# Kernel tuning notes

Hardware: AMD Instinct MI355X
Metric: run time of the kernel (lower is better)

## Reference

```python
import jax, jax.numpy as jnp
from jax import lax
import numpy as np

DIM = 256
D_STATE = 16
D_CONV = 4
EXPAND = 2
D_INNER = EXPAND * DIM          # 512
DT_RANK = (DIM + 15) // 16      # 16
EPS = 1e-5


def setup_inputs() -> dict:
    key = jax.random.key(0)
    ks = jax.random.split(key, 8)
    B, H, W = 8, 32, 32
    dt_init = 0.01  # softplus(b_dt) ~= dt_init at init (mamba-style)
    return {
        "x": jax.random.normal(ks[0], (B, DIM, H, W), jnp.float32),
        "ln_gamma": jnp.ones((DIM,), jnp.float32),
        "ln_beta": jnp.zeros((DIM,), jnp.float32),
        "W_in": jax.random.normal(ks[1], (DIM, 2 * D_INNER), jnp.float32) * 0.02,
        "conv_w": jax.random.normal(ks[2], (D_INNER, D_CONV), jnp.float32) * 0.2,
        "conv_b": jnp.zeros((D_INNER,), jnp.float32),
        "W_xproj": jax.random.normal(ks[3], (D_INNER, DT_RANK + 2 * D_STATE), jnp.float32) * 0.02,
        "W_dt": jax.random.normal(ks[4], (DT_RANK, D_INNER), jnp.float32) * 0.05,
        "b_dt": jnp.full((D_INNER,), float(np.log(np.expm1(dt_init))), jnp.float32),
        "A_log": jnp.log(jnp.broadcast_to(
            jnp.arange(1, D_STATE + 1, dtype=jnp.float32), (D_INNER, D_STATE))),
        "D_skip": jnp.ones((D_INNER,), jnp.float32),
        "W_out": jax.random.normal(ks[5], (D_INNER, DIM), jnp.float32) * 0.02,
    }


def _mamba_layer(x, ln_gamma, ln_beta, W_in, conv_w, conv_b, W_xproj,
                 W_dt, b_dt, A_log, D_skip, W_out):
    B, C, H, W = x.shape
    L = H * W
    # (B,C,H,W) -> (B, L, C)
    xf = x.transpose(0, 2, 3, 1).reshape(B, L, C)
    # LayerNorm over channel dim
    mu = xf.mean(-1, keepdims=True)
    var = ((xf - mu) ** 2).mean(-1, keepdims=True)
    xn = (xf - mu) * lax.rsqrt(var + EPS) * ln_gamma + ln_beta
    # in_proj -> u (ssm branch) and z (gate branch)
    xz = xn @ W_in                              # [B, L, 2*D_INNER]
    u, z = xz[..., :D_INNER], xz[..., D_INNER:]
    # causal depthwise conv1d over L, then SiLU
    uc = u.transpose(0, 2, 1)                   # [B, D_INNER, L]
    uc = lax.conv_general_dilated(
        uc, conv_w[:, None, :], window_strides=(1,),
        padding=[(D_CONV - 1, 0)], feature_group_count=D_INNER)
    u2 = jax.nn.silu(uc + conv_b[None, :, None]).transpose(0, 2, 1)  # [B, L, D_INNER]
    # input-dependent dt, B, C
    dbc = u2 @ W_xproj                          # [B, L, DT_RANK + 2*D_STATE]
    dt = jax.nn.softplus(dbc[..., :DT_RANK] @ W_dt + b_dt)            # [B, L, D_INNER]
    Bm = dbc[..., DT_RANK:DT_RANK + D_STATE]    # [B, L, D_STATE]
    Cm = dbc[..., DT_RANK + D_STATE:]           # [B, L, D_STATE]
    A = -jnp.exp(A_log)                         # [D_INNER, D_STATE]

    def step(h, ins):
        dt_t, B_t, C_t, u_t = ins               # [B,Din], [B,S], [B,S], [B,Din]
        dA = jnp.exp(dt_t[:, :, None] * A)      # [B, Din, S]
        h = dA * h + dt_t[:, :, None] * B_t[:, None, :] * u_t[:, :, None]
        y = jnp.einsum('bds,bs->bd', h, C_t)
        return h, y

    h0 = jnp.zeros((B, D_INNER, D_STATE), xf.dtype)
    xs = (dt.transpose(1, 0, 2), Bm.transpose(1, 0, 2),
          Cm.transpose(1, 0, 2), u2.transpose(1, 0, 2))
    _, ys = lax.scan(step, h0, xs)              # ys: [L, B, D_INNER]
    y = ys.transpose(1, 0, 2) + u2 * D_skip     # skip connection D*u
    y = y * jax.nn.silu(z)                      # gate
    o = y @ W_out                               # [B, L, C]
    return o.reshape(B, H, W, C).transpose(0, 3, 1, 2) + x


def reference(x, ln_gamma, ln_beta, W_in, conv_w, conv_b, W_xproj,
              W_dt, b_dt, A_log, D_skip, W_out):
    return _mamba_layer(x, ln_gamma, ln_beta, W_in, conv_w, conv_b, W_xproj,
                        W_dt, b_dt, A_log, D_skip, W_out)
```

## Files before the change

kernel.cpp:

```cpp
#include <hip/hip_runtime.h>
#include <hip/hip_bf16.h>
#include <math.h>

#define DIMC   256
#define DI     512
#define DS     16
#define DTR    16
#define NX     48
#define BATCH  8
#define LSEQ   1024
#define MROWS  8192
#define CHUNK  64
#define NC     (LSEQ / CHUNK)

typedef __attribute__((ext_vector_type(8))) short short8;
typedef __attribute__((ext_vector_type(4))) float f32x4;

__device__ __forceinline__ unsigned short f2bf(float v) {
  __hip_bfloat16 h = __float2bfloat16(v);
  return *reinterpret_cast<unsigned short*>(&h);
}
__device__ __forceinline__ float bf2f(unsigned short u) {
  return __int_as_float(((int)u) << 16);
}

__device__ __forceinline__ void load_lds16(const void* g, void* l) {
  __builtin_amdgcn_global_load_lds(
      (const __attribute__((address_space(1))) unsigned int*)g,
      (__attribute__((address_space(3))) unsigned int*)l, 16, 0, 0);
}

__device__ __forceinline__ float dpp_sum16(float v) {
  float t;
  t = __int_as_float(__builtin_amdgcn_mov_dpp(__float_as_int(v), 0xB1,  0xF, 0xF, true)); v += t;
  t = __int_as_float(__builtin_amdgcn_mov_dpp(__float_as_int(v), 0x4E,  0xF, 0xF, true)); v += t;
  t = __int_as_float(__builtin_amdgcn_mov_dpp(__float_as_int(v), 0x141, 0xF, 0xF, true)); v += t;
  t = __int_as_float(__builtin_amdgcn_mov_dpp(__float_as_int(v), 0x140, 0xF, 0xF, true)); v += t;
  return v;
}

__global__ __launch_bounds__(256) void prologue(const float* __restrict__ W_in,
                                                const float* __restrict__ W_out,
                                                const float* __restrict__ W_xproj,
                                                const float* __restrict__ W_dt,
                                                const float* __restrict__ x,
                                                const float* __restrict__ gamma,
                                                const float* __restrict__ beta,
                                                unsigned short* __restrict__ Wib,
                                                unsigned short* __restrict__ Wob,
                                                unsigned short* __restrict__ Wxpb,
                                                unsigned short* __restrict__ Wdtb,
                                                unsigned short* __restrict__ xnb) {
  __shared__ float sx[DIMC][67];
  __shared__ float smean[64], srs[64];
  const int blk = blockIdx.x, tid = threadIdx.x;
  if (blk < 384) {
    float (*t)[67] = sx;
    const float* W; unsigned short* Wt; int K, N, bx, by;
    if (blk < 256) { W = W_in;  Wt = Wib; K = DIMC; N = 1024; bx = blk & 31; by = blk >> 5; }
    else           { W = W_out; Wt = Wob; K = DI;   N = DIMC; bx = (blk - 256) & 7; by = (blk - 256) >> 3; }
    int n0 = bx * 32, k0 = by * 32;
    int tx = tid & 31, ty = tid >> 5;
    for (int i = ty; i < 32; i += 8) t[i][tx] = W[(size_t)(k0 + i) * N + n0 + tx];
    __syncthreads();
    for (int i = ty; i < 32; i += 8)
      Wt[(size_t)(n0 + i) * K + k0 + tx] = f2bf(t[tx][i]);
    return;
  }
  if (blk < 512) {
    int idx = (blk - 384) * 256 + tid;
    int n = idx >> 9, k = idx & 511;
    Wxpb[idx] = (n < NX) ? f2bf(W_xproj[(size_t)k * NX + n]) : (unsigned short)0;
    return;
  }
  if (blk < 576) {
    int idx = (blk - 512) * 256 + tid;
    int n = idx >> 5, k = idx & 31;
    Wdtb[idx] = (k < DTR) ? f2bf(W_dt[(size_t)k * DI + n]) : (unsigned short)0;
    return;
  }
  const int lb = blk - 576;
  const int b = lb >> 4, l0 = (lb & 15) * 64;
  {
    const int cbase = tid >> 2;
    const int lp = (tid & 3) * 16;
#pragma unroll
    for (int cg = 0; cg < 4; ++cg) {
      const int c = cg * 64 + cbase;
      const float* p = x + ((size_t)b * DIMC + c) * LSEQ + l0 + lp;
#pragma unroll
      for (int q = 0; q < 4; ++q) {
        float4 v = *(const float4*)(p + q * 4);
        sx[c][lp + q * 4 + 0] = v.x;
        sx[c][lp + q * 4 + 1] = v.y;
        sx[c][lp + q * 4 + 2] = v.z;
        sx[c][lp + q * 4 + 3] = v.w;
      }
    }
  }
  __syncthreads();
  {
    const int lane = tid & 63, w = tid >> 6;
    const int l = (w << 4) + (lane & 15);
    const int quad = lane >> 4;
    float sum = 0.f, sq = 0.f;
#pragma unroll 8
    for (int cc = 0; cc < 64; ++cc) {
      float v = sx[quad * 64 + cc][l];
      sum += v; sq += v * v;
    }
    sum += __shfl_xor(sum, 16); sq += __shfl_xor(sq, 16);
    sum += __shfl_xor(sum, 32); sq += __shfl_xor(sq, 32);
    if (quad == 0) {
      float mean = sum * (1.f / 256.f);
      float var  = sq * (1.f / 256.f) - mean * mean;
      smean[l] = mean; srs[l] = rsqrtf(var + 1e-5f);
    }
  }
  __syncthreads();
  {
    const float gg = gamma[tid], bb = beta[tid];
    const size_t base = ((size_t)b * LSEQ + l0) * DIMC + tid;
#pragma unroll 4
    for (int ll = 0; ll < 64; ++ll) {
      float v = (sx[tid][ll] - smean[ll]) * srs[ll] * gg + bb;
      xnb[base + (size_t)ll * DIMC] = f2bf(v);
    }
  }
}

__global__ __launch_bounds__(256) void gemm_bf16_128(const unsigned short* __restrict__ A,
                                                     const unsigned short* __restrict__ Bt,
                                                     unsigned short* __restrict__ Cb,
                                                     int M, int N, int K) {
  __shared__ unsigned short As[128][32];
  __shared__ unsigned short Bs[128][32];
  const int tid = threadIdx.x;
  const int lane = tid & 63, wave = tid >> 6;
  const int wm = wave >> 1, wn = wave & 1;
  const int quad = lane >> 4, l16 = lane & 15;
  const int m0 = blockIdx.y * 128, n0 = blockIdx.x * 128;

  f32x4 acc[4][4];
#pragma unroll
  for (int i = 0; i < 4; ++i)
#pragma unroll
    for (int j = 0; j < 4; ++j) acc[i][j] = (f32x4){0.f, 0.f, 0.f, 0.f};

  for (int k0 = 0; k0 < K; k0 += 32) {
#pragma unroll
    for (int q = 0; q < 2; ++q) {
      int id = q * 256 + tid;
      int row = id >> 2, c = id & 3;
      load_lds16(A + (size_t)(m0 + row) * K + k0 + c * 8,
                 (char*)&As[0][0] + (size_t)(q * 256 + wave * 64) * 16);
    }
#pragma unroll
    for (int q = 0; q < 2; ++q) {
      int id = q * 256 + tid;
      int row = id >> 2, c = id & 3;
      load_lds16(Bt + (size_t)(n0 + row) * K + k0 + c * 8,
                 (char*)&Bs[0][0] + (size_t)(q * 256 + wave * 64) * 16);
    }
    __syncthreads();
    short8 af[4], bfr[4];
#pragma unroll
    for (int i = 0; i < 4; ++i)
      af[i] = *(const short8*)&As[wm * 64 + i * 16 + l16][quad * 8];
#pragma unroll
    for (int j = 0; j < 4; ++j)
      bfr[j] = *(const short8*)&Bs[wn * 64 + j * 16 + l16][quad * 8];
#pragma unroll
    for (int i = 0; i < 4; ++i)
#pragma unroll
      for (int j = 0; j < 4; ++j)
        acc[i][j] = __builtin_amdgcn_mfma_f32_16x16x32_bf16(af[i], bfr[j], acc[i][j], 0, 0, 0);
    __syncthreads();
  }

#pragma unroll
  for (int i = 0; i < 4; ++i) {
    int rowb = wm * 64 + i * 16 + quad * 4;
#pragma unroll
    for (int j = 0; j < 4; ++j) {
      int n = n0 + wn * 64 + j * 16 + l16;
#pragma unroll
      for (int r = 0; r < 4; ++r)
        Cb[(size_t)(m0 + rowb + r) * N + n] = f2bf(acc[i][j][r]);
    }
  }
}

#define GTM 128
#define GTN 64
#define GBK 32
__global__ __launch_bounds__(256) void gemm_bf16(const unsigned short* __restrict__ A,
                                                 const unsigned short* __restrict__ Bt,
                                                 void* __restrict__ Cout,
                                                 int M, int N, int K, int mode,
                                                 const float* __restrict__ X) {
  __shared__ unsigned short As[GTM][GBK];
  __shared__ unsigned short Bs[GTN][GBK];
  const int tid = threadIdx.x;
  const int lane = tid & 63, wave = tid >> 6;
  const int wm = wave >> 1, wn = wave & 1;
  const int quad = lane >> 4, l16 = lane & 15;
  const int m0 = blockIdx.y * GTM, n0 = blockIdx.x * GTN;

  f32x4 acc[4][2];
#pragma unroll
  for (int i = 0; i < 4; ++i)
#pragma unroll
    for (int j = 0; j < 2; ++j) acc[i][j] = (f32x4){0.f, 0.f, 0.f, 0.f};

  for (int k0 = 0; k0 < K; k0 += GBK) {
#pragma unroll
    for (int q = 0; q < 2; ++q) {
      int id = q * 256 + tid;
      int row = id >> 2, c = id & 3;
      load_lds16(A + (size_t)(m0 + row) * K + k0 + c * 8,
                 (char*)&As[0][0] + (size_t)(q * 256 + wave * 64) * 16);
    }
    {
      int row = tid >> 2, c = tid & 3;
      load_lds16(Bt + (size_t)(n0 + row) * K + k0 + c * 8,
                 (char*)&Bs[0][0] + (size_t)(wave * 64) * 16);
    }
    __syncthreads();
    short8 af[4], bfrag[2];
#pragma unroll
    for (int i = 0; i < 4; ++i)
      af[i] = *(const short8*)&As[wm * 64 + i * 16 + l16][quad * 8];
#pragma unroll
    for (int j = 0; j < 2; ++j)
      bfrag[j] = *(const short8*)&Bs[wn * 32 + j * 16 + l16][quad * 8];
#pragma unroll
    for (int i = 0; i < 4; ++i)
#pragma unroll
      for (int j = 0; j < 2; ++j)
        acc[i][j] = __builtin_amdgcn_mfma_f32_16x16x32_bf16(af[i], bfrag[j], acc[i][j], 0, 0, 0);
    __syncthreads();
  }

  if (mode == 2) {
    unsigned short* Cb = (unsigned short*)Cout;
#pragma unroll
    for (int i = 0; i < 4; ++i) {
      int rowb = wm * 64 + i * 16 + quad * 4;
#pragma unroll
      for (int j = 0; j < 2; ++j) {
        int n = n0 + wn * 32 + j * 16 + l16;
#pragma unroll
        for (int r = 0; r < 4; ++r)
          Cb[(size_t)(m0 + rowb + r) * N + n] = f2bf(acc[i][j][r]);
      }
    }
  } else {
    float* C = (float*)Cout;
#pragma unroll
    for (int i = 0; i < 4; ++i) {
      int m = m0 + wm * 64 + i * 16 + quad * 4;
      int b = m >> 10, l = m & 1023;
#pragma unroll
      for (int j = 0; j < 2; ++j) {
        int n = n0 + wn * 32 + j * 16 + l16;
        size_t o = (size_t)b * (DIMC * LSEQ) + (size_t)n * LSEQ + l;
        f32x4 xv = *(const f32x4*)(X + o);
        f32x4 rv = acc[i][j] + xv;
        *(f32x4*)(C + o) = rv;
      }
    }
  }
}

__global__ __launch_bounds__(256) void conv_xproj_dt(
    const unsigned short* __restrict__ xzb,
    const float* __restrict__ conv_w,
    const float* __restrict__ conv_b,
    const unsigned short* __restrict__ Wxpb,
    const unsigned short* __restrict__ Wdtb,
    const float* __restrict__ b_dt,
    float* __restrict__ dbcBC,
    unsigned int* __restrict__ dtu) {
  __shared__ unsigned short sxz[19][512];
  __shared__ unsigned short su[16][512 + 8];
  __shared__ unsigned short sdbc[16][40];
  const int m0 = blockIdx.x * 16;
  const int l0 = m0 & 1023;
  const int tid = threadIdx.x, lane = tid & 63, w = tid >> 6;
  const int quad = lane >> 4, l16 = lane & 15;

#pragma unroll
  for (int q = 0; q < 5; ++q) {
    int id = q * 256 + tid;
    if (id < 19 * 64) {
      int rr = id >> 6, c8 = id & 63;
      uint4 v; v.x = 0u; v.y = 0u; v.z = 0u; v.w = 0u;
      if (l0 - 3 + rr >= 0)
        v = *(const uint4*)(xzb + (size_t)(m0 - 3 + rr) * 1024 + c8 * 8);
      *(uint4*)&sxz[rr][c8 * 8] = v;
    }
  }
  __syncthreads();

#pragma unroll 4
  for (int q = 0; q < 32; ++q) {
    int idx = q * 256 + tid;
    int r = idx >> 9, c = idx & 511;
    float4 wv = *(const float4*)(conv_w + c * 4);
    float acc = conv_b[c];
    acc = fmaf(bf2f(sxz[r + 0][c]), wv.x, acc);
    acc = fmaf(bf2f(sxz[r + 1][c]), wv.y, acc);
    acc = fmaf(bf2f(sxz[r + 2][c]), wv.z, acc);
    acc = fmaf(bf2f(sxz[r + 3][c]), wv.w, acc);
    float u = acc / (1.f + __expf(-acc));
    su[r][c] = f2bf(u);
  }
  __syncthreads();

  f32x4 acc = (f32x4){0.f, 0.f, 0.f, 0.f};
#pragma unroll 4
  for (int k0 = 0; k0 < 512; k0 += 32) {
    short8 af = *(const short8*)&su[l16][k0 + quad * 8];
    short8 bf = *(const short8*)(Wxpb + (size_t)(w * 16 + l16) * 512 + k0 + quad * 8);
    acc = __builtin_amdgcn_mfma_f32_16x16x32_bf16(af, bf, acc, 0, 0, 0);
  }
  if (w == 1 || w == 2) {
#pragma unroll
    for (int r = 0; r < 4; ++r)
      dbcBC[(size_t)(m0 + quad * 4 + r) * 32 + (w - 1) * 16 + l16] = acc[r];
  }
  if (w < 2) {
#pragma unroll
    for (int r = 0; r < 4; ++r)
      sdbc[quad * 4 + r][w * 16 + l16] = f2bf(acc[r]);
  }
  __syncthreads();

  short8 af0 = *(const short8*)&sdbc[l16][quad * 8];
#pragma unroll
  for (int jn = 0; jn < 8; ++jn) {
    const int n0 = w * 128 + jn * 16;
    short8 bf = *(const short8*)(Wdtb + (size_t)(n0 + l16) * 32 + quad * 8);
    f32x4 a0 = (f32x4){0.f, 0.f, 0.f, 0.f};
    a0 = __builtin_amdgcn_mfma_f32_16x16x32_bf16(af0, bf, a0, 0, 0, 0);
    const float bd = b_dt[n0 + l16];
#pragma unroll
    for (int r = 0; r < 4; ++r) {
      int lr0 = quad * 4 + r;
      float v = a0[r] + bd;
      float sp = (v > 20.f) ? v : log1pf(__expf(v));
      unsigned int u0 = (unsigned int)su[lr0][n0 + l16];
      dtu[(size_t)(m0 + lr0) * DI + n0 + l16] = u0 | ((unsigned int)f2bf(sp) << 16);
    }
  }
}

__global__ __launch_bounds__(256) void scan_pass1(const unsigned int* __restrict__ dtu,
                                                  const float* __restrict__ dbcBC,
                                                  const float* __restrict__ A_log,
                                                  float* __restrict__ hend,
                                                  float* __restrict__ Ssum) {
  const int bb = blockIdx.x, dblk = blockIdx.y, cc = blockIdx.z;
  const int tid = threadIdx.x;
  const int di = tid >> 4, s = tid & 15;
  const int d = dblk * 16 + di;
  const float Ads = -__expf(A_log[d * DS + s]);

  __shared__ float2 sdu[CHUNK][18];
  __shared__ float  sB[CHUNK][17];
  {
    const int t0 = cc * CHUNK;
    int lin = tid * 4;
    int tt = lin >> 4, dd = lin & 15;
    size_t m = (size_t)bb * LSEQ + t0 + tt;
    uint4 du4 = *(const uint4*)(dtu + m * DI + dblk * 16 + dd);
    f32x4 a, b2;
    a[0]  = bf2f((unsigned short)(du4.x >> 16)); a[1]  = bf2f((unsigned short)(du4.x & 0xffff));
    a[2]  = bf2f((unsigned short)(du4.y >> 16)); a[3]  = bf2f((unsigned short)(du4.y & 0xffff));
    b2[0] = bf2f((unsigned short)(du4.z >> 16)); b2[1] = bf2f((unsigned short)(du4.z & 0xffff));
    b2[2] = bf2f((unsigned short)(du4.w >> 16)); b2[3] = bf2f((unsigned short)(du4.w & 0xffff));
    *(f32x4*)&sdu[tt][dd]     = a;
    *(f32x4*)&sdu[tt][dd + 2] = b2;
    f32x4 Bv = *(const f32x4*)(dbcBC + m * 32 + dd);
    *(f32x4*)&sB[tt][dd] = Bv;
  }
  __syncthreads();
  float h = 0.f, dtsum = 0.f;
#pragma unroll 4
  for (int tt = 0; tt < CHUNK; ++tt) {
    float2 du = sdu[tt][di];
    float Bv  = sB[tt][s];
    h = fmaf(__expf(du.x * Ads), h, du.x * du.y * Bv);
    dtsum += du.x;
  }
  size_t ci = ((size_t)(bb * NC + cc) * DI + d);
  hend[ci * DS + s] = h;
  if (s == 0) Ssum[ci] = dtsum;
}

__global__ __launch_bounds__(256) void scan_pass2(const float* __restrict__ A_log,
                                                  const float* __restrict__ hend,
                                                  const float* __restrict__ Ssum,
                                                  float* __restrict__ hin) {
  const int bb = blockIdx.x, dblk = blockIdx.y;
  const int tid = threadIdx.x;
  const int di = tid >> 4, s = tid & 15;
  const int d = dblk * 16 + di;
  const float Ads = -__expf(A_log[d * DS + s]);
  float h = 0.f;
  for (int cc = 0; cc < NC; ++cc) {
    size_t ci = ((size_t)(bb * NC + cc) * DI + d);
    hin[ci * DS + s] = h;
    h = fmaf(__expf(Ads * Ssum[ci]), h, hend[ci * DS + s]);
  }
}

__global__ __launch_bounds__(256) void scan_pass3(const unsigned int* __restrict__ dtu,
                                                  const float* __restrict__ dbcBC,
                                                  const unsigned short* __restrict__ xzb,
                                                  const float* __restrict__ A_log,
                                                  const float* __restrict__ D_skip,
                                                  const float* __restrict__ hin,
                                                  unsigned short* __restrict__ yb) {
  const int bb = blockIdx.x, dblk = blockIdx.y, cc = blockIdx.z;
  const int tid = threadIdx.x;
  const int di = tid >> 4, s = tid & 15;
  const int d = dblk * 16 + di;
  const float Ads = -__expf(A_log[d * DS + s]);

  __shared__ float2 sdu[CHUNK][18];
  __shared__ float2 sBC[CHUNK][18];
  __shared__ float  sy[CHUNK][16];
  const int t0 = cc * CHUNK;
  const size_t mbase = (size_t)bb * LSEQ + t0;
  {
    int lin = tid * 4;
    int tt = lin >> 4, dd = lin & 15;
    size_t m = mbase + tt;
    uint4 du4 = *(const uint4*)(dtu + m * DI + dblk * 16 + dd);
    f32x4 a, b2;
    a[0]  = bf2f((unsigned short)(du4.x >> 16)); a[1]  = bf2f((unsigned short)(du4.x & 0xffff));
    a[2]  = bf2f((unsigned short)(du4.y >> 16)); a[3]  = bf2f((unsigned short)(du4.y & 0xffff));
    b2[0] = bf2f((unsigned short)(du4.z >> 16)); b2[1] = bf2f((unsigned short)(du4.z & 0xffff));
    b2[2] = bf2f((unsigned short)(du4.w >> 16)); b2[3] = bf2f((unsigned short)(du4.w & 0xffff));
    *(f32x4*)&sdu[tt][dd]     = a;
    *(f32x4*)&sdu[tt][dd + 2] = b2;
    f32x4 Bv = *(const f32x4*)(dbcBC + m * 32 + dd);
    f32x4 Cv = *(const f32x4*)(dbcBC + m * 32 + 16 + dd);
    f32x4 p0, p1;
    p0[0] = Bv[0]; p0[1] = Cv[0]; p0[2] = Bv[1]; p0[3] = Cv[1];
    p1[0] = Bv[2]; p1[1] = Cv[2]; p1[2] = Bv[3]; p1[3] = Cv[3];
    *(f32x4*)&sBC[tt][dd]     = p0;
    *(f32x4*)&sBC[tt][dd + 2] = p1;
  }
  __syncthreads();
  float h = hin[((size_t)(bb * NC + cc) * DI + d) * DS + s];
#pragma unroll 4
  for (int tt = 0; tt < CHUNK; ++tt) {
    float2 du = sdu[tt][di];
    float2 bc = sBC[tt][s];
    h = fmaf(__expf(du.x * Ads), h, du.x * du.y * bc.x);
    float v = dpp_sum16(h * bc.y);
    if (s == 0) sy[tt][di] = v;
  }
  __syncthreads();
#pragma unroll
  for (int q = 0; q < 4; ++q) {
    int lin = q * 256 + tid;
    int tt = lin >> 4, dd = lin & 15;
    size_t m = mbase + tt;
    float z = bf2f(xzb[m * 1024 + DI + dblk * 16 + dd]);
    float yv = sy[tt][dd] + sdu[tt][dd].y * D_skip[dblk * 16 + dd];
    yv *= z / (1.f + __expf(-z));
    yb[m * DI + dblk * 16 + dd] = f2bf(yv);
  }
}

extern "C" void kernel_launch(void* const* d_in, const int* in_sizes, int n_in,
                              void* d_out, int out_size, void* d_ws, size_t ws_size,
                              hipStream_t stream) {
  const float* x       = (const float*)d_in[0];
  const float* ln_g    = (const float*)d_in[1];
  const float* ln_b    = (const float*)d_in[2];
  const float* W_in    = (const float*)d_in[3];
  const float* conv_w  = (const float*)d_in[4];
  const float* conv_b  = (const float*)d_in[5];
  const float* W_xproj = (const float*)d_in[6];
  const float* W_dt    = (const float*)d_in[7];
  const float* b_dt    = (const float*)d_in[8];
  const float* A_log   = (const float*)d_in[9];
  const float* D_skip  = (const float*)d_in[10];
  const float* W_out   = (const float*)d_in[11];
  float* out = (float*)d_out;

  float* ws    = (float*)d_ws;
  float* dbcBC = ws;
  float* hend  = dbcBC + (size_t)MROWS * 32;
  float* hin   = hend + (size_t)BATCH * NC * DI * DS;
  float* Ssum  = hin  + (size_t)BATCH * NC * DI * DS;
  unsigned int* dtu = (unsigned int*)(Ssum + (size_t)BATCH * NC * DI);
  unsigned short* xzb  = (unsigned short*)(dtu + (size_t)MROWS * DI);
  unsigned short* yb   = xzb + (size_t)MROWS * 1024;
  unsigned short* xnb  = yb;
  unsigned short* Wib  = yb  + (size_t)MROWS * DI;
  unsigned short* Wob  = Wib + (size_t)DIMC * 1024;
  unsigned short* Wxpb = Wob + (size_t)DI * DIMC;
  unsigned short* Wdtb = Wxpb + (size_t)64 * 512;

  prologue<<<704, 256, 0, stream>>>(W_in, W_out, W_xproj, W_dt, x, ln_g, ln_b,
                                    Wib, Wob, Wxpb, Wdtb, xnb);

  gemm_bf16_128<<<dim3(1024 / 128, MROWS / 128), 256, 0, stream>>>(
      xnb, Wib, xzb, MROWS, 1024, DIMC);

  conv_xproj_dt<<<MROWS / 16, 256, 0, stream>>>(xzb, conv_w, conv_b,
                                                Wxpb, Wdtb, b_dt, dbcBC, dtu);

  dim3 gp13(BATCH, DI / 16, NC);
  dim3 gp2(BATCH, DI / 16);
  scan_pass1<<<gp13, 256, 0, stream>>>(dtu, dbcBC, A_log, hend, Ssum);
  scan_pass2<<<gp2, 256, 0, stream>>>(A_log, hend, Ssum, hin);
  scan_pass3<<<gp13, 256, 0, stream>>>(dtu, dbcBC, xzb, A_log, D_skip, hin, yb);

  gemm_bf16<<<dim3(DIMC / GTN, MROWS / GTM), 256, 0, stream>>>(
      yb, Wob, out, MROWS, DIMC, DI, 1, x);
}
```

Baseline: 185.4 us.

## Fuse three-pass chunked scan into one sequential double-buffered scan kernel

Replaces the chunked scan (chunk-end states, carry propagation, chunk rescan) with a single kernel where each block scans the whole sequence for 16 channels, prefetching the next 128-step tile into registers and double-buffered LDS. This removes the first pass's reread of dt/u/B, the intermediate state buffers and two launches. In exchange the grid shrinks to 256 blocks and each thread runs a 1024-step serial recurrence, reducing parallelism and latency hiding.

New measurement: 246.6 us. 33.0% more time.

```diff
diff --git a/kernel.cpp b/kernel.cpp
--- a/kernel.cpp
+++ b/kernel.cpp
@@ -12,6 +12,8 @@
 #define MROWS  8192
 #define CHUNK  64
 #define NC     (LSEQ / CHUNK)
+#define TCH    128
+#define NT     (LSEQ / TCH)
 
 typedef __attribute__((ext_vector_type(8))) short short8;
 typedef __attribute__((ext_vector_type(4))) float f32x4;
@@ -356,124 +358,97 @@
   }
 }
 
-__global__ __launch_bounds__(256) void scan_pass1(const unsigned int* __restrict__ dtu,
-                                                  const float* __restrict__ dbcBC,
-                                                  const float* __restrict__ A_log,
-                                                  float* __restrict__ hend,
-                                                  float* __restrict__ Ssum) {
-  const int bb = blockIdx.x, dblk = blockIdx.y, cc = blockIdx.z;
-  const int tid = threadIdx.x;
-  const int di = tid >> 4, s = tid & 15;
-  const int d = dblk * 16 + di;
-  const float Ads = -__expf(A_log[d * DS + s]);
-
-  __shared__ float2 sdu[CHUNK][18];
-  __shared__ float  sB[CHUNK][17];
-  {
-    const int t0 = cc * CHUNK;
-    int lin = tid * 4;
-    int tt = lin >> 4, dd = lin & 15;
-    size_t m = (size_t)bb * LSEQ + t0 + tt;
-    uint4 du4 = *(const uint4*)(dtu + m * DI + dblk * 16 + dd);
-    f32x4 a, b2;
-    a[0]  = bf2f((unsigned short)(du4.x >> 16)); a[1]  = bf2f((unsigned short)(du4.x & 0xffff));
-    a[2]  = bf2f((unsigned short)(du4.y >> 16)); a[3]  = bf2f((unsigned short)(du4.y & 0xffff));
-    b2[0] = bf2f((unsigned short)(du4.z >> 16)); b2[1] = bf2f((unsigned short)(du4.z & 0xffff));
-    b2[2] = bf2f((unsigned short)(du4.w >> 16)); b2[3] = bf2f((unsigned short)(du4.w & 0xffff));
-    *(f32x4*)&sdu[tt][dd]     = a;
-    *(f32x4*)&sdu[tt][dd + 2] = b2;
-    f32x4 Bv = *(const f32x4*)(dbcBC + m * 32 + dd);
-    *(f32x4*)&sB[tt][dd] = Bv;
-  }
-  __syncthreads();
-  float h = 0.f, dtsum = 0.f;
-#pragma unroll 4
-  for (int tt = 0; tt < CHUNK; ++tt) {
-    float2 du = sdu[tt][di];
-    float Bv  = sB[tt][s];
-    h = fmaf(__expf(du.x * Ads), h, du.x * du.y * Bv);
-    dtsum += du.x;
-  }
-  size_t ci = ((size_t)(bb * NC + cc) * DI + d);
-  hend[ci * DS + s] = h;
-  if (s == 0) Ssum[ci] = dtsum;
-}
-
-__global__ __launch_bounds__(256) void scan_pass2(const float* __restrict__ A_log,
-                                                  const float* __restrict__ hend,
-                                                  const float* __restrict__ Ssum,
-                                                  float* __restrict__ hin) {
+__device__ __forceinline__ void scan_stage_store(
+    float2 (*sdu)[TCH + 1], float2 (*sBC)[TCH + 1],
+    int sdd, int stt, uint4 ra, uint4 rb,
+    f32x4 vB0, f32x4 vB1, f32x4 vC0, f32x4 vC1) {
+  unsigned int wv[8] = {ra.x, ra.y, ra.z, ra.w, rb.x, rb.y, rb.z, rb.w};
+  float Bv[8] = {vB0[0], vB0[1], vB0[2], vB0[3], vB1[0], vB1[1], vB1[2], vB1[3]};
+  float Cv[8] = {vC0[0], vC0[1], vC0[2], vC0[3], vC1[0], vC1[1], vC1[2], vC1[3]};
+#pragma unroll
+  for (int j = 0; j < 8; ++j) {
+    sdu[sdd + j][stt] = make_float2(bf2f((unsigned short)(wv[j] >> 16)),
+                                    bf2f((unsigned short)(wv[j] & 0xffff)));
+    sBC[sdd + j][stt] = make_float2(Bv[j], Cv[j]);
+  }
+}
+
+__global__ __launch_bounds__(256) void scan_fused(
+    const unsigned int* __restrict__ dtu,
+    const float* __restrict__ dbcBC,
+    const unsigned short* __restrict__ xzb,
+    const float* __restrict__ A_log,
+    const float* __restrict__ D_skip,
+    unsigned short* __restrict__ yb) {
   const int bb = blockIdx.x, dblk = blockIdx.y;
   const int tid = threadIdx.x;
   const int di = tid >> 4, s = tid & 15;
   const int d = dblk * 16 + di;
   const float Ads = -__expf(A_log[d * DS + s]);
+
+  __shared__ float2 sdu[2][16][TCH + 1];
+  __shared__ float2 sBC[2][16][TCH + 1];
+  __shared__ float  sy[TCH][16];
+
+  const int stt = tid >> 1;
+  const int sdd = (tid & 1) * 8;
+  const size_t brow = (size_t)bb * LSEQ;
+
+  uint4 ra, rb;
+  f32x4 vB0, vB1, vC0, vC1;
+
+  {
+    size_t m = brow + stt;
+    const unsigned int* pdu = dtu + m * DI + dblk * 16 + sdd;
+    ra = *(const uint4*)pdu;
+    rb = *(const uint4*)(pdu + 4);
+    const float* pbc = dbcBC + m * 32 + sdd;
+    vB0 = *(const f32x4*)pbc;
+    vB1 = *(const f32x4*)(pbc + 4);
+    vC0 = *(const f32x4*)(pbc + 16);
+    vC1 = *(const f32x4*)(pbc + 20);
+  }
+  scan_stage_store(sdu[0], sBC[0], sdd, stt, ra, rb, vB0, vB1, vC0, vC1);
+  __syncthreads();
+
   float h = 0.f;
-  for (int cc = 0; cc < NC; ++cc) {
-    size_t ci = ((size_t)(bb * NC + cc) * DI + d);
-    hin[ci * DS + s] = h;
-    h = fmaf(__expf(Ads * Ssum[ci]), h, hend[ci * DS + s]);
-  }
-}
-
-__global__ __launch_bounds__(256) void scan_pass3(const unsigned int* __restrict__ dtu,
-                                                  const float* __restrict__ dbcBC,
-                                                  const unsigned short* __restrict__ xzb,
-                                                  const float* __restrict__ A_log,
-                                                  const float* __restrict__ D_skip,
-                                                  const float* __restrict__ hin,
-                                                  unsigned short* __restrict__ yb) {
-  const int bb = blockIdx.x, dblk = blockIdx.y, cc = blockIdx.z;
-  const int tid = threadIdx.x;
-  const int di = tid >> 4, s = tid & 15;
-  const int d = dblk * 16 + di;
-  const float Ads = -__expf(A_log[d * DS + s]);
-
-  __shared__ float2 sdu[CHUNK][18];
-  __shared__ float2 sBC[CHUNK][18];
-  __shared__ float  sy[CHUNK][16];
-  const int t0 = cc * CHUNK;
-  const size_t mbase = (size_t)bb * LSEQ + t0;
-  {
-    int lin = tid * 4;
-    int tt = lin >> 4, dd = lin & 15;
-    size_t m = mbase + tt;
-    uint4 du4 = *(const uint4*)(dtu + m * DI + dblk * 16 + dd);
-    f32x4 a, b2;
-    a[0]  = bf2f((unsigned short)(du4.x >> 16)); a[1]  = bf2f((unsigned short)(du4.x & 0xffff));
-    a[2]  = bf2f((unsigned short)(du4.y >> 16)); a[3]  = bf2f((unsigned short)(du4.y & 0xffff));
-    b2[0] = bf2f((unsigned short)(du4.z >> 16)); b2[1] = bf2f((unsigned short)(du4.z & 0xffff));
-    b2[2] = bf2f((unsigned short)(du4.w >> 16)); b2[3] = bf2f((unsigned short)(du4.w & 0xffff));
-    *(f32x4*)&sdu[tt][dd]     = a;
-    *(f32x4*)&sdu[tt][dd + 2] = b2;
-    f32x4 Bv = *(const f32x4*)(dbcBC + m * 32 + dd);
-    f32x4 Cv = *(const f32x4*)(dbcBC + m * 32 + 16 + dd);
-    f32x4 p0, p1;
-    p0[0] = Bv[0]; p0[1] = Cv[0]; p0[2] = Bv[1]; p0[3] = Cv[1];
-    p1[0] = Bv[2]; p1[1] = Cv[2]; p1[2] = Bv[3]; p1[3] = Cv[3];
-    *(f32x4*)&sBC[tt][dd]     = p0;
-    *(f32x4*)&sBC[tt][dd + 2] = p1;
-  }
-  __syncthreads();
-  float h = hin[((size_t)(bb * NC + cc) * DI + d) * DS + s];
-#pragma unroll 4
-  for (int tt = 0; tt < CHUNK; ++tt) {
-    float2 du = sdu[tt][di];
-    float2 bc = sBC[tt][s];
-    h = fmaf(__expf(du.x * Ads), h, du.x * du.y * bc.x);
-    float v = dpp_sum16(h * bc.y);
-    if (s == 0) sy[tt][di] = v;
-  }
-  __syncthreads();
-#pragma unroll
-  for (int q = 0; q < 4; ++q) {
-    int lin = q * 256 + tid;
-    int tt = lin >> 4, dd = lin & 15;
-    size_t m = mbase + tt;
-    float z = bf2f(xzb[m * 1024 + DI + dblk * 16 + dd]);
-    float yv = sy[tt][dd] + sdu[tt][dd].y * D_skip[dblk * 16 + dd];
-    yv *= z / (1.f + __expf(-z));
-    yb[m * DI + dblk * 16 + dd] = f2bf(yv);
+  int buf = 0;
+  for (int tile = 0; tile < NT; ++tile) {
+    if (tile + 1 < NT) {
+      size_t m = brow + (size_t)(tile + 1) * TCH + stt;
+      const unsigned int* pdu = dtu + m * DI + dblk * 16 + sdd;
+      ra = *(const uint4*)pdu;
+      rb = *(const uint4*)(pdu + 4);
+      const float* pbc = dbcBC + m * 32 + sdd;
+      vB0 = *(const f32x4*)pbc;
+      vB1 = *(const f32x4*)(pbc + 4);
+      vC0 = *(const f32x4*)(pbc + 16);
+      vC1 = *(const f32x4*)(pbc + 20);
+    }
+#pragma unroll 8
+    for (int tt = 0; tt < TCH; ++tt) {
+      float2 du = sdu[buf][di][tt];
+      float2 bc = sBC[buf][s][tt];
+      h = fmaf(__expf(du.x * Ads), h, du.x * du.y * bc.x);
+      float v = dpp_sum16(h * bc.y);
+      if (s == 0) sy[tt][di] = v;
+    }
+    __syncthreads();
+#pragma unroll
+    for (int q = 0; q < 8; ++q) {
+      int lin = q * 256 + tid;
+      int tt = lin >> 4, dd = lin & 15;
+      size_t m = brow + (size_t)tile * TCH + tt;
+      float z = bf2f(xzb[m * 1024 + DI + dblk * 16 + dd]);
+      float u = sdu[buf][dd][tt].y;
+      float yv = sy[tt][dd] + u * D_skip[dblk * 16 + dd];
+      yv *= z / (1.f + __expf(-z));
+      yb[m * DI + dblk * 16 + dd] = f2bf(yv);
+    }
+    if (tile + 1 < NT)
+      scan_stage_store(sdu[buf ^ 1], sBC[buf ^ 1], sdd, stt, ra, rb, vB0, vB1, vC0, vC1);
+    __syncthreads();
+    buf ^= 1;
   }
 }
 
@@ -507,6 +482,7 @@
   unsigned short* Wob  = Wib + (size_t)DIMC * 1024;
   unsigned short* Wxpb = Wob + (size_t)DI * DIMC;
   unsigned short* Wdtb = Wxpb + (size_t)64 * 512;
+  (void)hend; (void)hin; (void)Ssum;
 
   prologue<<<704, 256, 0, stream>>>(W_in, W_out, W_xproj, W_dt, x, ln_g, ln_b,
                                     Wib, Wob, Wxpb, Wdtb, xnb);
@@ -517,11 +493,8 @@
   conv_xproj_dt<<<MROWS / 16, 256, 0, stream>>>(xzb, conv_w, conv_b,
                                                 Wxpb, Wdtb, b_dt, dbcBC, dtu);
 
-  dim3 gp13(BATCH, DI / 16, NC);
-  dim3 gp2(BATCH, DI / 16);
-  scan_pass1<<<gp13, 256, 0, stream>>>(dtu, dbcBC, A_log, hend, Ssum);
-  scan_pass2<<<gp2, 256, 0, stream>>>(A_log, hend, Ssum, hin);
-  scan_pass3<<<gp13, 256, 0, stream>>>(dtu, dbcBC, xzb, A_log, D_skip, hin, yb);
+  scan_fused<<<dim3(BATCH, DI / 16), 256, 0, stream>>>(dtu, dbcBC, xzb,
+                                                       A_log, D_skip, yb);
 
   gemm_bf16<<<dim3(DIMC / GTN, MROWS / GTM), 256, 0, stream>>>(
       yb, Wob, out, MROWS, DIMC, DI, 1, x);
```

## Replace three-pass chunked scan with local scan plus linear correction pass

Applied to the files above, without the earlier changes.

The three scan kernels (local chunk end states, a serial cross-chunk pass, then a rescan with carried state) become two. The first kernel scans each chunk from zero state and writes the local output with the skip term, per-step cumulative dt sums, and end states. The second rebuilds each chunk's incoming state from earlier chunks' end states and adds a correction C·exp(A·S)·h_in before the gate. This removes the small serial pass2 launch and the second sequential recurrence, at the cost of writing and re-reading two extra fp32 MROWS×DI buffers (Scum, yloc).

Result: slower. 201.7 us (+8.7%).

```diff
diff --git a/kernel.cpp b/kernel.cpp
--- a/kernel.cpp
+++ b/kernel.cpp
@@ -356,11 +356,13 @@
   }
 }
 
-__global__ __launch_bounds__(256) void scan_pass1(const unsigned int* __restrict__ dtu,
+__global__ __launch_bounds__(256) void scan_local(const unsigned int* __restrict__ dtu,
                                                   const float* __restrict__ dbcBC,
                                                   const float* __restrict__ A_log,
+                                                  const float* __restrict__ D_skip,
                                                   float* __restrict__ hend,
-                                                  float* __restrict__ Ssum) {
+                                                  float* __restrict__ Scum,
+                                                  float* __restrict__ yloc) {
   const int bb = blockIdx.x, dblk = blockIdx.y, cc = blockIdx.z;
   const int tid = threadIdx.x;
   const int di = tid >> 4, s = tid & 15;
@@ -368,69 +370,8 @@
   const float Ads = -__expf(A_log[d * DS + s]);
 
   __shared__ float2 sdu[CHUNK][18];
-  __shared__ float  sB[CHUNK][17];
-  {
-    const int t0 = cc * CHUNK;
-    int lin = tid * 4;
-    int tt = lin >> 4, dd = lin & 15;
-    size_t m = (size_t)bb * LSEQ + t0 + tt;
-    uint4 du4 = *(const uint4*)(dtu + m * DI + dblk * 16 + dd);
-    f32x4 a, b2;
-    a[0]  = bf2f((unsigned short)(du4.x >> 16)); a[1]  = bf2f((unsigned short)(du4.x & 0xffff));
-    a[2]  = bf2f((unsigned short)(du4.y >> 16)); a[3]  = bf2f((unsigned short)(du4.y & 0xffff));
-    b2[0] = bf2f((unsigned short)(du4.z >> 16)); b2[1] = bf2f((unsigned short)(du4.z & 0xffff));
-    b2[2] = bf2f((unsigned short)(du4.w >> 16)); b2[3] = bf2f((unsigned short)(du4.w & 0xffff));
-    *(f32x4*)&sdu[tt][dd]     = a;
-    *(f32x4*)&sdu[tt][dd + 2] = b2;
-    f32x4 Bv = *(const f32x4*)(dbcBC + m * 32 + dd);
-    *(f32x4*)&sB[tt][dd] = Bv;
-  }
-  __syncthreads();
-  float h = 0.f, dtsum = 0.f;
-#pragma unroll 4
-  for (int tt = 0; tt < CHUNK; ++tt) {
-    float2 du = sdu[tt][di];
-    float Bv  = sB[tt][s];
-    h = fmaf(__expf(du.x * Ads), h, du.x * du.y * Bv);
-    dtsum += du.x;
-  }
-  size_t ci = ((size_t)(bb * NC + cc) * DI + d);
-  hend[ci * DS + s] = h;
-  if (s == 0) Ssum[ci] = dtsum;
-}
-
-__global__ __launch_bounds__(256) void scan_pass2(const float* __restrict__ A_log,
-                                                  const float* __restrict__ hend,
-                                                  const float* __restrict__ Ssum,
-                                                  float* __restrict__ hin) {
-  const int bb = blockIdx.x, dblk = blockIdx.y;
-  const int tid = threadIdx.x;
-  const int di = tid >> 4, s = tid & 15;
-  const int d = dblk * 16 + di;
-  const float Ads = -__expf(A_log[d * DS + s]);
-  float h = 0.f;
-  for (int cc = 0; cc < NC; ++cc) {
-    size_t ci = ((size_t)(bb * NC + cc) * DI + d);
-    hin[ci * DS + s] = h;
-    h = fmaf(__expf(Ads * Ssum[ci]), h, hend[ci * DS + s]);
-  }
-}
-
-__global__ __launch_bounds__(256) void scan_pass3(const unsigned int* __restrict__ dtu,
-                                                  const float* __restrict__ dbcBC,
-                                                  const unsigned short* __restrict__ xzb,
-                                                  const float* __restrict__ A_log,
-                                                  const float* __restrict__ D_skip,
-                                                  const float* __restrict__ hin,
-                                                  unsigned short* __restrict__ yb) {
-  const int bb = blockIdx.x, dblk = blockIdx.y, cc = blockIdx.z;
-  const int tid = threadIdx.x;
-  const int di = tid >> 4, s = tid & 15;
-  const int d = dblk * 16 + di;
-  const float Ads = -__expf(A_log[d * DS + s]);
-
-  __shared__ float2 sdu[CHUNK][18];
   __shared__ float2 sBC[CHUNK][18];
+  __shared__ float  sS[CHUNK][17];
   __shared__ float  sy[CHUNK][16];
   const int t0 = cc * CHUNK;
   const size_t mbase = (size_t)bb * LSEQ + t0;
@@ -455,13 +396,74 @@
     *(f32x4*)&sBC[tt][dd + 2] = p1;
   }
   __syncthreads();
-  float h = hin[((size_t)(bb * NC + cc) * DI + d) * DS + s];
+  const float Dsk = D_skip[d];
+  float h = 0.f, dts = 0.f;
 #pragma unroll 4
   for (int tt = 0; tt < CHUNK; ++tt) {
     float2 du = sdu[tt][di];
     float2 bc = sBC[tt][s];
+    dts += du.x;
     h = fmaf(__expf(du.x * Ads), h, du.x * du.y * bc.x);
     float v = dpp_sum16(h * bc.y);
+    if (s == 0) { sy[tt][di] = fmaf(du.y, Dsk, v); sS[tt][di] = dts; }
+  }
+  __syncthreads();
+  hend[((size_t)(bb * NC + cc) * DI + d) * DS + s] = h;
+#pragma unroll
+  for (int q = 0; q < 4; ++q) {
+    int lin = q * 256 + tid;
+    int tt = lin >> 4, dd = lin & 15;
+    size_t m = mbase + tt;
+    Scum[m * DI + dblk * 16 + dd] = sS[tt][dd];
+    yloc[m * DI + dblk * 16 + dd] = sy[tt][dd];
+  }
+}
+
+__global__ __launch_bounds__(256) void scan_fix(const float* __restrict__ dbcBC,
+                                                const unsigned short* __restrict__ xzb,
+                                                const float* __restrict__ A_log,
+                                                const float* __restrict__ D_skip,
+                                                const float* __restrict__ hend,
+                                                const float* __restrict__ Scum,
+                                                const float* __restrict__ yloc,
+                                                unsigned short* __restrict__ yb) {
+  const int bb = blockIdx.x, dblk = blockIdx.y, cc = blockIdx.z;
+  const int tid = threadIdx.x;
+  const int di = tid >> 4, s = tid & 15;
+  const int d = dblk * 16 + di;
+  const float Ads = -__expf(A_log[d * DS + s]);
+  const int t0 = cc * CHUNK;
+  const size_t mbase = (size_t)bb * LSEQ + t0;
+
+  __shared__ float sC[16][CHUNK + 1];
+  __shared__ float sS[16][CHUNK + 1];
+  __shared__ float sy[CHUNK][16];
+
+#pragma unroll
+  for (int q = 0; q < 4; ++q) {
+    int lin = q * 256 + tid;
+    int tt = lin >> 4, ee = lin & 15;
+    size_t m = mbase + tt;
+    sC[ee][tt] = dbcBC[m * 32 + 16 + ee];
+    sS[ee][tt] = Scum[m * DI + dblk * 16 + ee];
+  }
+
+  float Stj[NC - 1], he[NC - 1];
+#pragma unroll
+  for (int j = 0; j < NC - 1; ++j) {
+    Stj[j] = Scum[((size_t)bb * LSEQ + j * CHUNK + CHUNK - 1) * DI + d];
+    he[j]  = hend[((size_t)(bb * NC + j) * DI + d) * DS + s];
+  }
+  float h = 0.f;
+#pragma unroll
+  for (int j = 0; j < NC - 1; ++j)
+    if (j < cc) h = fmaf(__expf(Ads * Stj[j]), h, he[j]);
+
+  __syncthreads();
+#pragma unroll 4
+  for (int tt = 0; tt < CHUNK; ++tt) {
+    float corr = sC[s][tt] * __expf(Ads * sS[di][tt]) * h;
+    float v = dpp_sum16(corr);
     if (s == 0) sy[tt][di] = v;
   }
   __syncthreads();
@@ -471,7 +473,7 @@
     int tt = lin >> 4, dd = lin & 15;
     size_t m = mbase + tt;
     float z = bf2f(xzb[m * 1024 + DI + dblk * 16 + dd]);
-    float yv = sy[tt][dd] + sdu[tt][dd].y * D_skip[dblk * 16 + dd];
+    float yv = yloc[m * DI + dblk * 16 + dd] + sy[tt][dd];
     yv *= z / (1.f + __expf(-z));
     yb[m * DI + dblk * 16 + dd] = f2bf(yv);
   }
@@ -507,6 +509,9 @@
   unsigned short* Wob  = Wib + (size_t)DIMC * 1024;
   unsigned short* Wxpb = Wob + (size_t)DI * DIMC;
   unsigned short* Wdtb = Wxpb + (size_t)64 * 512;
+  float* Scum = (float*)(Wdtb + (size_t)512 * 32);
+  float* yloc = Scum + (size_t)MROWS * DI;
+  (void)hin; (void)Ssum;
 
   prologue<<<704, 256, 0, stream>>>(W_in, W_out, W_xproj, W_dt, x, ln_g, ln_b,
                                     Wib, Wob, Wxpb, Wdtb, xnb);
@@ -517,11 +522,11 @@
   conv_xproj_dt<<<MROWS / 16, 256, 0, stream>>>(xzb, conv_w, conv_b,
                                                 Wxpb, Wdtb, b_dt, dbcBC, dtu);
 
-  dim3 gp13(BATCH, DI / 16, NC);
-  dim3 gp2(BATCH, DI / 16);
-  scan_pass1<<<gp13, 256, 0, stream>>>(dtu, dbcBC, A_log, hend, Ssum);
-  scan_pass2<<<gp2, 256, 0, stream>>>(A_log, hend, Ssum, hin);
-  scan_pass3<<<gp13, 256, 0, stream>>>(dtu, dbcBC, xzb, A_log, D_skip, hin, yb);
+  dim3 gsc(BATCH, DI / 16, NC);
+  scan_local<<<gsc, 256, 0, stream>>>(dtu, dbcBC, A_log, D_skip,
+                                      hend, Scum, yloc);
+  scan_fix<<<gsc, 256, 0, stream>>>(dbcBC, xzb, A_log, D_skip,
+                                    hend, Scum, yloc, yb);
 
   gemm_bf16<<<dim3(DIMC / GTN, MROWS / GTM), 256, 0, stream>>>(
       yb, Wob, out, MROWS, DIMC, DI, 1, x);
```

## Remap chunked scan to one channel per thread with register-held states

Applied to the files above, without the earlier changes.

Scan pass 1 and pass 3 now give each thread one inner channel and keep all 16 state values in registers, instead of spreading the 16 states of a channel across 16 lanes. This drops the DPP cross-lane reduction and the shared-memory staging of dt/u and y, and reads dtu, z and writes y directly with coalesced per-channel accesses. The chunk size is halved to 32, which doubles the number of chunks and the length of the sequential carry pass in scan_pass2. Each thread now does 16 exps per step, so there is less parallelism per block and more register pressure.

Result: no change. 185.9 us (+0.3%).

```diff
diff --git a/kernel.cpp b/kernel.cpp
--- a/kernel.cpp
+++ b/kernel.cpp
@@ -10,7 +10,7 @@
 #define BATCH  8
 #define LSEQ   1024
 #define MROWS  8192
-#define CHUNK  64
+#define CHUNK  32
 #define NC     (LSEQ / CHUNK)
 
 typedef __attribute__((ext_vector_type(8))) short short8;
@@ -28,15 +28,6 @@
   __builtin_amdgcn_global_load_lds(
       (const __attribute__((address_space(1))) unsigned int*)g,
       (__attribute__((address_space(3))) unsigned int*)l, 16, 0, 0);
-}
-
-__device__ __forceinline__ float dpp_sum16(float v) {
-  float t;
-  t = __int_as_float(__builtin_amdgcn_mov_dpp(__float_as_int(v), 0xB1,  0xF, 0xF, true)); v += t;
-  t = __int_as_float(__builtin_amdgcn_mov_dpp(__float_as_int(v), 0x4E,  0xF, 0xF, true)); v += t;
-  t = __int_as_float(__builtin_amdgcn_mov_dpp(__float_as_int(v), 0x141, 0xF, 0xF, true)); v += t;
-  t = __int_as_float(__builtin_amdgcn_mov_dpp(__float_as_int(v), 0x140, 0xF, 0xF, true)); v += t;
-  return v;
 }
 
 __global__ __launch_bounds__(256) void prologue(const float* __restrict__ W_in,
@@ -361,42 +352,57 @@
                                                   const float* __restrict__ A_log,
                                                   float* __restrict__ hend,
                                                   float* __restrict__ Ssum) {
-  const int bb = blockIdx.x, dblk = blockIdx.y, cc = blockIdx.z;
+  const int bb = blockIdx.x, dh = blockIdx.y, cc = blockIdx.z;
   const int tid = threadIdx.x;
-  const int di = tid >> 4, s = tid & 15;
-  const int d = dblk * 16 + di;
-  const float Ads = -__expf(A_log[d * DS + s]);
-
-  __shared__ float2 sdu[CHUNK][18];
-  __shared__ float  sB[CHUNK][17];
+  const int d = dh * 256 + tid;
+
+  __shared__ float sB[CHUNK][16];
+  const size_t mbase = (size_t)bb * LSEQ + cc * CHUNK;
+#pragma unroll
+  for (int q = 0; q < 2; ++q) {
+    int lin = q * 256 + tid;
+    int tt = lin >> 4, ss = lin & 15;
+    sB[tt][ss] = dbcBC[(mbase + tt) * 32 + ss];
+  }
+
+  float Ads[16];
   {
-    const int t0 = cc * CHUNK;
-    int lin = tid * 4;
-    int tt = lin >> 4, dd = lin & 15;
-    size_t m = (size_t)bb * LSEQ + t0 + tt;
-    uint4 du4 = *(const uint4*)(dtu + m * DI + dblk * 16 + dd);
-    f32x4 a, b2;
-    a[0]  = bf2f((unsigned short)(du4.x >> 16)); a[1]  = bf2f((unsigned short)(du4.x & 0xffff));
-    a[2]  = bf2f((unsigned short)(du4.y >> 16)); a[3]  = bf2f((unsigned short)(du4.y & 0xffff));
-    b2[0] = bf2f((unsigned short)(du4.z >> 16)); b2[1] = bf2f((unsigned short)(du4.z & 0xffff));
-    b2[2] = bf2f((unsigned short)(du4.w >> 16)); b2[3] = bf2f((unsigned short)(du4.w & 0xffff));
-    *(f32x4*)&sdu[tt][dd]     = a;
-    *(f32x4*)&sdu[tt][dd + 2] = b2;
-    f32x4 Bv = *(const f32x4*)(dbcBC + m * 32 + dd);
-    *(f32x4*)&sB[tt][dd] = Bv;
-  }
-  __syncthreads();
-  float h = 0.f, dtsum = 0.f;
+    const f32x4* pa = (const f32x4*)(A_log + (size_t)d * DS);
+#pragma unroll
+    for (int q = 0; q < 4; ++q) {
+      f32x4 v = pa[q];
+#pragma unroll
+      for (int r = 0; r < 4; ++r) Ads[q * 4 + r] = -__expf(v[r]);
+    }
+  }
+  __syncthreads();
+
+  float h[16];
+#pragma unroll
+  for (int s = 0; s < 16; ++s) h[s] = 0.f;
+  float dts = 0.f;
+  const unsigned int* pdu = dtu + mbase * DI + d;
 #pragma unroll 4
   for (int tt = 0; tt < CHUNK; ++tt) {
-    float2 du = sdu[tt][di];
-    float Bv  = sB[tt][s];
-    h = fmaf(__expf(du.x * Ads), h, du.x * du.y * Bv);
-    dtsum += du.x;
-  }
-  size_t ci = ((size_t)(bb * NC + cc) * DI + d);
-  hend[ci * DS + s] = h;
-  if (s == 0) Ssum[ci] = dtsum;
+    unsigned int wv = pdu[(size_t)tt * DI];
+    float dt = bf2f((unsigned short)(wv >> 16));
+    float u  = bf2f((unsigned short)(wv & 0xffff));
+    dts += dt;
+    float c = dt * u;
+#pragma unroll
+    for (int s = 0; s < 16; ++s)
+      h[s] = fmaf(__expf(dt * Ads[s]), h[s], c * sB[tt][s]);
+  }
+  const size_t ci = (size_t)(bb * NC + cc) * DI + d;
+  f32x4* ph = (f32x4*)(hend + ci * DS);
+#pragma unroll
+  for (int q = 0; q < 4; ++q) {
+    f32x4 v;
+#pragma unroll
+    for (int r = 0; r < 4; ++r) v[r] = h[q * 4 + r];
+    ph[q] = v;
+  }
+  Ssum[ci] = dts;
 }
 
 __global__ __launch_bounds__(256) void scan_pass2(const float* __restrict__ A_log,
@@ -409,6 +415,7 @@
   const int d = dblk * 16 + di;
   const float Ads = -__expf(A_log[d * DS + s]);
   float h = 0.f;
+#pragma unroll 4
   for (int cc = 0; cc < NC; ++cc) {
     size_t ci = ((size_t)(bb * NC + cc) * DI + d);
     hin[ci * DS + s] = h;
@@ -423,57 +430,63 @@
                                                   const float* __restrict__ D_skip,
                                                   const float* __restrict__ hin,
                                                   unsigned short* __restrict__ yb) {
-  const int bb = blockIdx.x, dblk = blockIdx.y, cc = blockIdx.z;
+  const int bb = blockIdx.x, dh = blockIdx.y, cc = blockIdx.z;
   const int tid = threadIdx.x;
-  const int di = tid >> 4, s = tid & 15;
-  const int d = dblk * 16 + di;
-  const float Ads = -__expf(A_log[d * DS + s]);
-
-  __shared__ float2 sdu[CHUNK][18];
-  __shared__ float2 sBC[CHUNK][18];
-  __shared__ float  sy[CHUNK][16];
-  const int t0 = cc * CHUNK;
-  const size_t mbase = (size_t)bb * LSEQ + t0;
+  const int d = dh * 256 + tid;
+
+  __shared__ float sB[CHUNK][16];
+  __shared__ float sC[CHUNK][16];
+  const size_t mbase = (size_t)bb * LSEQ + cc * CHUNK;
+#pragma unroll
+  for (int q = 0; q < 2; ++q) {
+    int lin = q * 256 + tid;
+    int tt = lin >> 4, ss = lin & 15;
+    sB[tt][ss] = dbcBC[(mbase + tt) * 32 + ss];
+    sC[tt][ss] = dbcBC[(mbase + tt) * 32 + 16 + ss];
+  }
+
+  float Ads[16];
   {
-    int lin = tid * 4;
-    int tt = lin >> 4, dd = lin & 15;
-    size_t m = mbase + tt;
-    uint4 du4 = *(const uint4*)(dtu + m * DI + dblk * 16 + dd);
-    f32x4 a, b2;
-    a[0]  = bf2f((unsigned short)(du4.x >> 16)); a[1]  = bf2f((unsigned short)(du4.x & 0xffff));
-    a[2]  = bf2f((unsigned short)(du4.y >> 16)); a[3]  = bf2f((unsigned short)(du4.y & 0xffff));
-    b2[0] = bf2f((unsigned short)(du4.z >> 16)); b2[1] = bf2f((unsigned short)(du4.z & 0xffff));
-    b2[2] = bf2f((unsigned short)(du4.w >> 16)); b2[3] = bf2f((unsigned short)(du4.w & 0xffff));
-    *(f32x4*)&sdu[tt][dd]     = a;
-    *(f32x4*)&sdu[tt][dd + 2] = b2;
-    f32x4 Bv = *(const f32x4*)(dbcBC + m * 32 + dd);
-    f32x4 Cv = *(const f32x4*)(dbcBC + m * 32 + 16 + dd);
-    f32x4 p0, p1;
-    p0[0] = Bv[0]; p0[1] = Cv[0]; p0[2] = Bv[1]; p0[3] = Cv[1];
-    p1[0] = Bv[2]; p1[1] = Cv[2]; p1[2] = Bv[3]; p1[3] = Cv[3];
-    *(f32x4*)&sBC[tt][dd]     = p0;
-    *(f32x4*)&sBC[tt][dd + 2] = p1;
-  }
-  __syncthreads();
-  float h = hin[((size_t)(bb * NC + cc) * DI + d) * DS + s];
+    const f32x4* pa = (const f32x4*)(A_log + (size_t)d * DS);
+#pragma unroll
+    for (int q = 0; q < 4; ++q) {
+      f32x4 v = pa[q];
+#pragma unroll
+      for (int r = 0; r < 4; ++r) Ads[q * 4 + r] = -__expf(v[r]);
+    }
+  }
+
+  float h[16];
+  {
+    const f32x4* ph = (const f32x4*)(hin + ((size_t)(bb * NC + cc) * DI + d) * DS);
+#pragma unroll
+    for (int q = 0; q < 4; ++q) {
+      f32x4 v = ph[q];
+#pragma unroll
+      for (int r = 0; r < 4; ++r) h[q * 4 + r] = v[r];
+    }
+  }
+  __syncthreads();
+
+  const float Dsk = D_skip[d];
+  const unsigned int* pdu = dtu + mbase * DI + d;
+  const unsigned short* pz = xzb + mbase * 1024 + DI + d;
+  unsigned short* py = yb + mbase * DI + d;
 #pragma unroll 4
   for (int tt = 0; tt < CHUNK; ++tt) {
-    float2 du = sdu[tt][di];
-    float2 bc = sBC[tt][s];
-    h = fmaf(__expf(du.x * Ads), h, du.x * du.y * bc.x);
-    float v = dpp_sum16(h * bc.y);
-    if (s == 0) sy[tt][di] = v;
-  }
-  __syncthreads();
-#pragma unroll
-  for (int q = 0; q < 4; ++q) {
-    int lin = q * 256 + tid;
-    int tt = lin >> 4, dd = lin & 15;
-    size_t m = mbase + tt;
-    float z = bf2f(xzb[m * 1024 + DI + dblk * 16 + dd]);
-    float yv = sy[tt][dd] + sdu[tt][dd].y * D_skip[dblk * 16 + dd];
-    yv *= z / (1.f + __expf(-z));
-    yb[m * DI + dblk * 16 + dd] = f2bf(yv);
+    unsigned int wv = pdu[(size_t)tt * DI];
+    float dt = bf2f((unsigned short)(wv >> 16));
+    float u  = bf2f((unsigned short)(wv & 0xffff));
+    float c = dt * u;
+    float y = u * Dsk;
+#pragma unroll
+    for (int s = 0; s < 16; ++s) {
+      h[s] = fmaf(__expf(dt * Ads[s]), h[s], c * sB[tt][s]);
+      y = fmaf(h[s], sC[tt][s], y);
+    }
+    float z = bf2f(pz[(size_t)tt * 1024]);
+    y *= z / (1.f + __expf(-z));
+    py[(size_t)tt * DI] = f2bf(y);
   }
 }
 
@@ -517,7 +530,7 @@
   conv_xproj_dt<<<MROWS / 16, 256, 0, stream>>>(xzb, conv_w, conv_b,
                                                 Wxpb, Wdtb, b_dt, dbcBC, dtu);
 
-  dim3 gp13(BATCH, DI / 16, NC);
+  dim3 gp13(BATCH, 2, NC);
   dim3 gp2(BATCH, DI / 16);
   scan_pass1<<<gp13, 256, 0, stream>>>(dtu, dbcBC, A_log, hend, Ssum);
   scan_pass2<<<gp2, 256, 0, stream>>>(A_log, hend, Ssum, hin);
```
